# Performance work log

Measured on AMD Instinct MI355X. Metric: run time of the kernel, lower is better.

Reference implementation:

```python
import jax, jax.numpy as jnp
import numpy as np
from jax import lax

D_MODEL = 1024
D_STATE = 128
HEADDIM = 64
EXPAND = 2
NGROUPS = 1
CHUNK = 256
D_INNER = EXPAND * D_MODEL          # 2048
D_SSM = D_INNER                      # d_ssm defaults to d_inner
NHEADS = D_SSM // HEADDIM            # 32
CONV_DIM = D_SSM + 2 * NGROUPS * D_STATE   # 2304
D_IN_PROJ = 2 * D_INNER + 2 * NGROUPS * D_STATE + NHEADS  # 4384 -> d_mlp = 0
BATCH = 2
SEQLEN = 2048
EPS = 1e-5


def setup_inputs() -> dict:
    key = jax.random.key(0)
    ks = jax.random.split(key, 9)
    u = jax.random.normal(ks[0], (BATCH, SEQLEN, D_MODEL), jnp.float32)
    # indices into left-padded (len = SEQLEN+1) sequence; 0 selects the zero pad
    conv_indices = jax.random.randint(ks[1], (BATCH, 4 * SEQLEN), 0, SEQLEN + 1)
    W_in = jax.random.normal(ks[2], (D_IN_PROJ, D_MODEL), jnp.float32) / np.sqrt(D_MODEL).astype(np.float32)
    conv_w = jax.random.normal(ks[3], (CONV_DIM, 4), jnp.float32) * 0.2
    conv_b = jax.random.normal(ks[4], (CONV_DIM,), jnp.float32) * 0.02
    # dt_bias init exactly as the module: inverse-softplus of dt in [dt_min, dt_max]
    dt = jnp.exp(jax.random.uniform(ks[5], (NHEADS,), jnp.float32) * (np.log(0.1) - np.log(0.001)) + np.log(0.001))
    dt = jnp.clip(dt, 1e-4)
    dt_bias = dt + jnp.log(-jnp.expm1(-dt))
    A_log = jnp.log(jax.random.uniform(ks[6], (NHEADS,), jnp.float32, minval=1.0, maxval=16.0))
    D = jnp.ones((NHEADS,), jnp.float32)
    norm_w = jnp.ones((D_SSM,), jnp.float32)
    W_out = jax.random.normal(ks[7], (D_MODEL, D_INNER), jnp.float32) / np.sqrt(D_INNER).astype(np.float32)
    return dict(u=u, conv_indices=conv_indices, W_in=W_in, conv_w=conv_w, conv_b=conv_b,
                dt_bias=dt_bias, A_log=A_log, D=D, norm_w=norm_w, W_out=W_out)


def _segsum(x):
    # x: (b, c, h, cs) -> (b, c, h, cs, cs); out[..., t, s] = sum_{k=s+1..t} x[..., k]
    cs = x.shape[-1]
    cx = jnp.cumsum(x, axis=-1)
    diff = cx[..., :, None] - cx[..., None, :]
    mask = jnp.tril(jnp.ones((cs, cs), dtype=bool))
    return jnp.where(mask, diff, -jnp.inf)


def _ssd(x, dt, A, Bh, Ch, D):
    # Mamba2 SSD chunked scan. x:(b,l,h,p), dt:(b,l,h), A:(h,), Bh/Ch:(b,l,h,n), D:(h,)
    b, l, h, p = x.shape
    n = Bh.shape[-1]
    c = l // CHUNK
    xr = x.reshape(b, c, CHUNK, h, p)
    dtr = dt.reshape(b, c, CHUNK, h)
    Br = Bh.reshape(b, c, CHUNK, h, n)
    Cr = Ch.reshape(b, c, CHUNK, h, n)
    dA = dtr * A                                 # (b,c,cs,h)
    Acum = jnp.cumsum(dA, axis=2)                # (b,c,cs,h)
    Lm = jnp.exp(_segsum(jnp.transpose(dA, (0, 1, 3, 2))))  # (b,c,h,cs,cs)
    dtx = xr * dtr[..., None]                    # dt-weighted inputs
    # intra-chunk (diagonal blocks)
    Yd = jnp.einsum('bcthn,bcshn,bchts,bcshp->bcthp', Cr, Br, Lm, dtx)
    # per-chunk final states
    decay_states = jnp.exp(Acum[:, :, -1:, :] - Acum)        # (b,c,cs,h)
    states = jnp.einsum('bcshn,bcsh,bcshp->bchpn', Br, decay_states, dtx)
    chunk_decay = jnp.exp(Acum[:, :, -1, :])     # (b,c,h)
    def step(h_prev, inp):
        dec, st = inp
        return h_prev * dec[..., None, None] + st, h_prev
    init = jnp.zeros((b, h, p, n), x.dtype)
    _, prev = lax.scan(step, init, (jnp.moveaxis(chunk_decay, 1, 0), jnp.moveaxis(states, 1, 0)))
    prev = jnp.moveaxis(prev, 0, 1)              # (b,c,h,p,n): state entering each chunk
    # inter-chunk (off-diagonal) contribution
    Yoff = jnp.einsum('bcthn,bchpn,bcth->bcthp', Cr, prev, jnp.exp(Acum))
    Y = Yd + Yoff + D[None, None, None, :, None] * xr
    return Y.reshape(b, l, h, p)


def reference(u, conv_indices, W_in, conv_w, conv_b, dt_bias, A_log, D, norm_w, W_out):
    b, l, _ = u.shape
    zxbcdt = u @ W_in.T                          # (b,l,4384); d_mlp == 0
    z, xBC, dt_raw = jnp.split(zxbcdt, [D_SSM, D_SSM + CONV_DIM], axis=-1)
    # tree conv: left-pad seq by 1, gather 4 tree positions per output step, depthwise conv k=4 stride=4
    xc = jnp.transpose(xBC, (0, 2, 1))           # (b, conv_dim, l)
    xp = jnp.pad(xc, ((0, 0), (0, 0), (1, 0)))
    idx = jnp.broadcast_to(conv_indices[:, None, :], (b, CONV_DIM, 4 * l))
    g = jnp.take_along_axis(xp, idx, axis=2).reshape(b, CONV_DIM, l, 4)
    conv = jnp.einsum('bclk,ck->bcl', g, conv_w) + conv_b[None, :, None]
    xBC = jax.nn.silu(jnp.transpose(conv, (0, 2, 1)))  # (b,l,conv_dim)
    x, Bm, Cm = jnp.split(xBC, [D_SSM, D_SSM + NGROUPS * D_STATE], axis=-1)
    x = x.reshape(b, l, NHEADS, HEADDIM)
    hpg = NHEADS // NGROUPS
    Bh = jnp.repeat(Bm.reshape(b, l, NGROUPS, D_STATE), hpg, axis=2)
    Ch = jnp.repeat(Cm.reshape(b, l, NGROUPS, D_STATE), hpg, axis=2)
    dt = jax.nn.softplus(dt_raw + dt_bias)       # dt_softplus=True, default dt_limit
    A = -jnp.exp(A_log.astype(jnp.float32))
    y = _ssd(x, dt, A, Bh, Ch, D).reshape(b, l, D_SSM)
    # RMSNormGated, norm_before_gate=False, group_size = d_ssm (ngroups=1)
    yz = y * jax.nn.silu(z)
    var = jnp.mean(jnp.square(yz), axis=-1, keepdims=True)
    y = yz * lax.rsqrt(var + EPS) * norm_w
    return y @ W_out.T
```

## Files before the change

### kernel.cpp

```cpp
#include <hip/hip_runtime.h>

#define BB 2
#define LL 2048
#define DMODEL 1024
#define DSSM 2048
#define NH 32
#define HD 64
#define DST 128
#define CONVD 2304
#define DPROJ 4384
#define CS 64
#define NC 32
#define BLTOT (BB*LL)

typedef short v8s __attribute__((ext_vector_type(8)));
typedef float v4f __attribute__((ext_vector_type(4)));

__device__ __forceinline__ float b2f(unsigned short h) {
  union { unsigned int u; float f; } v; v.u = ((unsigned int)h) << 16; return v.f;
}
__device__ __forceinline__ unsigned short f2b(float f) {
  union { float f; unsigned int u; } v; v.f = f;
  unsigned int u = v.u;
  return (unsigned short)((u + 0x7fffu + ((u >> 16) & 1u)) >> 16);
}
__device__ __forceinline__ v4f mfma16(v8s a, v8s b, v4f c) {
  return __builtin_amdgcn_mfma_f32_16x16x32_bf16(a, b, c, 0, 0, 0);
}
__device__ __forceinline__ void gl_lds16(const unsigned short* g, unsigned short* l) {
  __builtin_amdgcn_global_load_lds(
      (const __attribute__((address_space(1))) void*)(g),
      (__attribute__((address_space(3))) void*)(l), 16, 0, 0);
}

__global__ __launch_bounds__(256) void cvt3_kernel(
    const float* __restrict__ a, unsigned short* __restrict__ oa, int na4,
    const float* __restrict__ b, unsigned short* __restrict__ ob, int nb4,
    const float* __restrict__ c, unsigned short* __restrict__ oc, int nc4)
{
  int i = blockIdx.x * 256 + threadIdx.x;
  const float* src; unsigned short* dst; int j;
  if (i < na4) { src = a; dst = oa; j = i; }
  else if (i < na4 + nb4) { src = b; dst = ob; j = i - na4; }
  else if (i < na4 + nb4 + nc4) { src = c; dst = oc; j = i - na4 - nb4; }
  else return;
  float4 v = ((const float4*)src)[j];
  ushort4 o;
  o.x = f2b(v.x); o.y = f2b(v.y); o.z = f2b(v.z); o.w = f2b(v.w);
  ((ushort4*)dst)[j] = o;
}

template<int TN, int OUT_BF16>
__global__ __launch_bounds__(256) void gemm_bt(
    const unsigned short* __restrict__ A, const unsigned short* __restrict__ Bt,
    void* __restrict__ Cout, int M, int N, int K, int ldc)
{
  constexpr int NT = TN / 32;
  const int bm = blockIdx.x, bn = blockIdx.y;
  const int tid = threadIdx.x;
  const int wave = tid >> 6, lane = tid & 63;
  const int wm = wave & 1, wn = wave >> 1;
  const int q = lane >> 4, lr = lane & 15;

  __shared__ __align__(16) unsigned short smem[128 * 64 + TN * 64];
  unsigned short* As = smem;
  unsigned short* Bs = smem + 128 * 64;

  v4f acc[4][NT];
#pragma unroll
  for (int i = 0; i < 4; i++)
#pragma unroll
    for (int j = 0; j < NT; j++) acc[i][j] = v4f{0.f, 0.f, 0.f, 0.f};

  const int lrow = lane >> 3;
  const int gchunk = (lane & 7) ^ lrow;

  for (int k0 = 0; k0 < K; k0 += 64) {
    __syncthreads();
#pragma unroll
    for (int it = 0; it < 4; ++it) {
      int r = wave * 32 + it * 8 + lrow;
      gl_lds16(A + (size_t)(bm * 128 + r) * K + k0 + gchunk * 8,
               &As[(wave * 32 + it * 8) * 64]);
    }
#pragma unroll
    for (int it = 0; it < TN / 32; ++it) {
      int rloc = wave * (TN / 4) + it * 8;
      int rb = bn * TN + rloc + lrow; if (rb >= N) rb = N - 1;
      gl_lds16(Bt + (size_t)rb * K + k0 + gchunk * 8, &Bs[rloc * 64]);
    }
    __syncthreads();
#pragma unroll
    for (int ks = 0; ks < 64; ks += 32) {
      const int c0 = (ks >> 3) + q;
      v8s af[4], bf[NT];
#pragma unroll
      for (int mt = 0; mt < 4; ++mt) {
        int r = wm * 64 + mt * 16 + lr;
        af[mt] = *(const v8s*)&As[r * 64 + ((c0 ^ (r & 7)) << 3)];
      }
#pragma unroll
      for (int nt = 0; nt < NT; ++nt) {
        int r = wn * (TN / 2) + nt * 16 + lr;
        bf[nt] = *(const v8s*)&Bs[r * 64 + ((c0 ^ (r & 7)) << 3)];
      }
#pragma unroll
      for (int mt = 0; mt < 4; ++mt)
#pragma unroll
        for (int nt = 0; nt < NT; ++nt)
          acc[mt][nt] = mfma16(af[mt], bf[nt], acc[mt][nt]);
    }
  }

  if constexpr (OUT_BF16) {
    __syncthreads();
    unsigned short* Cs = smem;
#pragma unroll
    for (int mt = 0; mt < 4; ++mt) {
#pragma unroll
      for (int nt = 0; nt < NT; ++nt) {
        int col = wn * (TN / 2) + nt * 16 + lr;
#pragma unroll
        for (int r = 0; r < 4; ++r) {
          int row = wm * 64 + mt * 16 + q * 4 + r;
          int baddr = (row * (TN * 2) + col * 2) ^ ((row & 7) << 4);
          *(unsigned short*)((char*)Cs + baddr) = f2b(acc[mt][nt][r]);
        }
      }
    }
    __syncthreads();
    constexpr int CHR = TN / 8;
#pragma unroll
    for (int u = tid; u < 128 * CHR; u += 256) {
      int row = u / CHR, ch = u % CHR;
      int baddr = row * (TN * 2) + ((ch ^ (row & 7)) << 4);
      uint4 v = *(const uint4*)((const char*)Cs + baddr);
      int gcol = bn * TN + ch * 8;
      if (gcol < N)
        *(uint4*)((unsigned short*)Cout + (size_t)(bm * 128 + row) * ldc + gcol) = v;
    }
  } else {
#pragma unroll
    for (int mt = 0; mt < 4; ++mt) {
#pragma unroll
      for (int nt = 0; nt < NT; ++nt) {
        int row = bm * 128 + wm * 64 + mt * 16 + q * 4;
        int col = bn * TN + wn * (TN / 2) + nt * 16 + lr;
        if (col < N) {
#pragma unroll
          for (int r = 0; r < 4; ++r)
            ((float*)Cout)[(size_t)(row + r) * ldc + col] = acc[mt][nt][r];
        }
      }
    }
  }
}

__global__ __launch_bounds__(256) void convBC_kernel(
    const unsigned short* __restrict__ C1, const int* __restrict__ cidx,
    const float* __restrict__ convw, const float* __restrict__ convb,
    const float* __restrict__ dtbias,
    unsigned short* __restrict__ Bg16, unsigned short* __restrict__ Cg16,
    float* __restrict__ dtb)
{
  int bl0 = blockIdx.x * 16;
  int b = bl0 >> 11;
  int tid = threadIdx.x;
  __shared__ int idxs[64];
  if (tid < 64) {
    int tk = tid >> 2, k = tid & 3;
    idxs[tid] = cidx[b * (4 * LL) + (((bl0 + tk) & 2047) * 4) + k];
  }
  __syncthreads();
  const float4* cw4 = (const float4*)convw;
  int quad = tid & 63;
  int relc = DSSM + quad * 4;
  float4 w0 = cw4[relc], w1 = cw4[relc + 1], w2 = cw4[relc + 2], w3 = cw4[relc + 3];
  float4 cb = *(const float4*)(convb + relc);
  int tk0 = (tid >> 6) * 4;
#pragma unroll
  for (int tt = 0; tt < 4; ++tt) {
    int tk = tk0 + tt;
    int bl = bl0 + tk;
    ushort4 rv[4];
#pragma unroll
    for (int k = 0; k < 4; ++k) {
      int iv = idxs[tk * 4 + k];
      rv[k] = (iv > 0) ? *(const ushort4*)(C1 + (size_t)(b * LL + iv - 1) * DPROJ + DSSM + relc)
                       : make_ushort4(0, 0, 0, 0);
    }
    float a0 = cb.x + b2f(rv[0].x) * w0.x + b2f(rv[1].x) * w0.y + b2f(rv[2].x) * w0.z + b2f(rv[3].x) * w0.w;
    float a1 = cb.y + b2f(rv[0].y) * w1.x + b2f(rv[1].y) * w1.y + b2f(rv[2].y) * w1.z + b2f(rv[3].y) * w1.w;
    float a2 = cb.z + b2f(rv[0].z) * w2.x + b2f(rv[1].z) * w2.y + b2f(rv[2].z) * w2.z + b2f(rv[3].z) * w2.w;
    float a3 = cb.w + b2f(rv[0].w) * w3.x + b2f(rv[1].w) * w3.y + b2f(rv[2].w) * w3.z + b2f(rv[3].w) * w3.w;
    ushort4 o;
    o.x = f2b(a0 / (1.f + __expf(-a0)));
    o.y = f2b(a1 / (1.f + __expf(-a1)));
    o.z = f2b(a2 / (1.f + __expf(-a2)));
    o.w = f2b(a3 / (1.f + __expf(-a3)));
    int cc = relc - DSSM;
    if (cc < DST) *(ushort4*)(Bg16 + (size_t)bl * DST + cc) = o;
    else          *(ushort4*)(Cg16 + (size_t)bl * DST + (cc - DST)) = o;
  }
  for (int u = tid; u < 16 * NH; u += 256) {
    int tk = u >> 5, hh = u & 31;
    int bl = bl0 + tk;
    float raw = b2f(C1[(size_t)bl * DPROJ + DSSM + CONVD + hh]) + dtbias[hh];
    float dtv = (raw > 20.f) ? raw : log1pf(__expf(raw));
    dtb[(size_t)bl * NH + hh] = dtv;
  }
}

__global__ __launch_bounds__(256) void d1_intra(
    const unsigned short* __restrict__ C1, const int* __restrict__ cidx,
    const float* __restrict__ convw, const float* __restrict__ convb,
    const unsigned short* __restrict__ Bg16,
    const unsigned short* __restrict__ Cg16, const float* __restrict__ dtb,
    const float* __restrict__ A_log, const float* __restrict__ Dp,
    unsigned short* __restrict__ y16, unsigned short* __restrict__ statesb,
    float* __restrict__ cdb, float* __restrict__ acumb)
{
  int gid = blockIdx.x;
  int h = gid & 31, ci = (gid >> 5) & 31, b = gid >> 10;
  int tid = threadIdx.x, wave = tid >> 6, lane = tid & 63, q = lane >> 4, lr = lane & 15;

  __shared__ __align__(16) unsigned short BnG[CS * 136];
  __shared__ __align__(16) unsigned short BTw[DST * 72];
  __shared__ __align__(16) unsigned short xT[HD * 72];
  __shared__ float dt_s[CS], ac_s[CS], dec_s[CS];
  __shared__ int idxs[CS * 4];
  __shared__ float wls[HD * 4];
  __shared__ float bls[HD];

  const size_t blbase = (size_t)b * LL + ci * CS;
  const size_t chbase = (size_t)(b * NC + ci) * NH + h;
  float Ah = -__expf(A_log[h]);

  if (wave == 0) {
    float d = dtb[(blbase + lane) * NH + h];
    float a = d * Ah;
#pragma unroll
    for (int off = 1; off < 64; off <<= 1) {
      float u = __shfl_up(a, off, 64);
      if (lane >= off) a += u;
    }
    float tot = __shfl(a, 63, 64);
    dt_s[lane] = d;
    ac_s[lane] = a;
    dec_s[lane] = __expf(tot - a);
    acumb[chbase * CS + lane] = a;
    if (lane == 0) cdb[chbase] = __expf(tot);
  }

#pragma unroll
  for (int g = 0; g < 8; ++g) {
    int f = g * 256 + tid;
    int s = f >> 5, c4 = (f & 31) * 4;
    *(ushort4*)&BnG[s * 136 + c4] = *(const ushort4*)(Bg16 + (blbase + s) * DST + c4);
  }
  {
    int s = tid >> 2, k = tid & 3;
    idxs[tid] = cidx[b * (4 * LL) + (ci * CS + s) * 4 + k];
  }
  if (tid < HD) *(float4*)&wls[tid * 4] = *(const float4*)(convw + (h * HD + tid) * 4);
  if (tid < HD / 4) *(float4*)&bls[tid * 4] = *(const float4*)(convb + h * HD + tid * 4);
  __syncthreads();

#pragma unroll
  for (int g = 0; g < 4; ++g) {
    int f = g * 256 + tid;
    int n = f >> 3, sg = f & 7;
    int s0 = sg * 8;
    ushort4 lo, hi;
    lo.x = f2b(b2f(BnG[(s0 + 0) * 136 + n]) * dec_s[s0 + 0] * dt_s[s0 + 0]);
    lo.y = f2b(b2f(BnG[(s0 + 1) * 136 + n]) * dec_s[s0 + 1] * dt_s[s0 + 1]);
    lo.z = f2b(b2f(BnG[(s0 + 2) * 136 + n]) * dec_s[s0 + 2] * dt_s[s0 + 2]);
    lo.w = f2b(b2f(BnG[(s0 + 3) * 136 + n]) * dec_s[s0 + 3] * dt_s[s0 + 3]);
    hi.x = f2b(b2f(BnG[(s0 + 4) * 136 + n]) * dec_s[s0 + 4] * dt_s[s0 + 4]);
    hi.y = f2b(b2f(BnG[(s0 + 5) * 136 + n]) * dec_s[s0 + 5] * dt_s[s0 + 5]);
    hi.z = f2b(b2f(BnG[(s0 + 6) * 136 + n]) * dec_s[s0 + 6] * dt_s[s0 + 6]);
    hi.w = f2b(b2f(BnG[(s0 + 7) * 136 + n]) * dec_s[s0 + 7] * dt_s[s0 + 7]);
    *(ushort4*)&BTw[n * 72 + s0] = lo;
    *(ushort4*)&BTw[n * 72 + s0 + 4] = hi;
  }

  v4f accS[4];
#pragma unroll
  for (int i = 0; i < 4; i++) accS[i] = v4f{0.f, 0.f, 0.f, 0.f};
#pragma unroll
  for (int ks = 0; ks < 128; ks += 32) {
    v8s a = *(const v8s*)(Cg16 + (blbase + wave * 16 + lr) * DST + ks + q * 8);
#pragma unroll
    for (int si = 0; si < 4; ++si) {
      v8s bb = *(const v8s*)&BnG[(si * 16 + lr) * 136 + ks + q * 8];
      accS[si] = mfma16(a, bb, accS[si]);
    }
  }

#pragma unroll
  for (int g = 0; g < 4; ++g) {
    int f = g * 256 + tid;
    int s = f >> 4, p4 = (f & 15) * 4;
    ushort4 rv[4];
#pragma unroll
    for (int k = 0; k < 4; ++k) {
      int iv = idxs[s * 4 + k];
      rv[k] = (iv > 0) ? *(const ushort4*)(C1 + (size_t)(b * LL + iv - 1) * DPROJ + DSSM + h * HD + p4)
                       : make_ushort4(0, 0, 0, 0);
    }
    float4 w0 = *(const float4*)&wls[(p4 + 0) * 4];
    float4 w1 = *(const float4*)&wls[(p4 + 1) * 4];
    float4 w2 = *(const float4*)&wls[(p4 + 2) * 4];
    float4 w3 = *(const float4*)&wls[(p4 + 3) * 4];
    float a0 = bls[p4 + 0] + b2f(rv[0].x) * w0.x + b2f(rv[1].x) * w0.y + b2f(rv[2].x) * w0.z + b2f(rv[3].x) * w0.w;
    float a1 = bls[p4 + 1] + b2f(rv[0].y) * w1.x + b2f(rv[1].y) * w1.y + b2f(rv[2].y) * w1.z + b2f(rv[3].y) * w1.w;
    float a2 = bls[p4 + 2] + b2f(rv[0].z) * w2.x + b2f(rv[1].z) * w2.y + b2f(rv[2].z) * w2.z + b2f(rv[3].z) * w2.w;
    float a3 = bls[p4 + 3] + b2f(rv[0].w) * w3.x + b2f(rv[1].w) * w3.y + b2f(rv[2].w) * w3.z + b2f(rv[3].w) * w3.w;
    xT[(p4 + 0) * 72 + s] = f2b(a0 / (1.f + __expf(-a0)));
    xT[(p4 + 1) * 72 + s] = f2b(a1 / (1.f + __expf(-a1)));
    xT[(p4 + 2) * 72 + s] = f2b(a2 / (1.f + __expf(-a2)));
    xT[(p4 + 3) * 72 + s] = f2b(a3 / (1.f + __expf(-a3)));
  }
  __syncthreads();

  {
    int tbase = wave * 16 + q * 4;
#pragma unroll
    for (int si = 0; si < 4; ++si) {
      int s = si * 16 + lr;
      float ds = dt_s[s], as = ac_s[s];
#pragma unroll
      for (int r = 0; r < 4; ++r) {
        int tt = tbase + r;
        float g = 0.f;
        if (s <= tt) g = accS[si][r] * __expf(ac_s[tt] - as) * ds;
        BnG[tt * 72 + s] = f2b(g);
      }
    }
  }
  __syncthreads();

  v4f accY[4], accPT[4][2];
#pragma unroll
  for (int i = 0; i < 4; i++) {
    accY[i] = v4f{0.f,0.f,0.f,0.f};
    accPT[i][0] = v4f{0.f,0.f,0.f,0.f};
    accPT[i][1] = v4f{0.f,0.f,0.f,0.f};
  }
  int nw = wave * 32;
#pragma unroll
  for (int ks = 0; ks < 64; ks += 32) {
    v8s xf[4];
#pragma unroll
    for (int i = 0; i < 4; ++i) xf[i] = *(const v8s*)&xT[(i * 16 + lr) * 72 + ks + q * 8];
    v8s aG  = *(const v8s*)&BnG[(wave * 16 + lr) * 72 + ks + q * 8];
    v8s bw0 = *(const v8s*)&BTw[(nw + lr) * 72 + ks + q * 8];
    v8s bw1 = *(const v8s*)&BTw[(nw + 16 + lr) * 72 + ks + q * 8];
#pragma unroll
    for (int nt = 0; nt < 4; ++nt) {
      accY[nt] = mfma16(aG, xf[nt], accY[nt]);
      accPT[nt][0] = mfma16(xf[nt], bw0, accPT[nt][0]);
      accPT[nt][1] = mfma16(xf[nt], bw1, accPT[nt][1]);
    }
  }

  float Dh = Dp[h];
#pragma unroll
  for (int nt = 0; nt < 4; ++nt) {
    int p = nt * 16 + lr;
#pragma unroll
    for (int r = 0; r < 4; ++r) {
      int t = wave * 16 + q * 4 + r;
      float xv = b2f(xT[p * 72 + t]);
      y16[(blbase + t) * DSSM + h * HD + p] = f2b(accY[nt][r] + Dh * xv);
    }
  }
  size_t sbase = chbase * (DST * HD);
#pragma unroll
  for (int mt = 0; mt < 4; ++mt) {
#pragma unroll
    for (int nt = 0; nt < 2; ++nt) {
      int n = nw + nt * 16 + lr;
#pragma unroll
      for (int r = 0; r < 4; ++r) {
        int p = mt * 16 + q * 4 + r;
        statesb[sbase + (size_t)p * DST + n] = f2b(accPT[mt][nt][r]);
      }
    }
  }
}

__global__ __launch_bounds__(256) void d2_scan(
    unsigned short* __restrict__ statesb, const float* __restrict__ cdb)
{
  int g = blockIdx.x;
  int seg = g & 31, bh = g >> 5;
  int b = bh >> 5, h = bh & 31;
  int e = seg * 256 + threadIdx.x;
  const size_t cstride = (size_t)NH * DST * HD;
  size_t base = ((size_t)(b * NC) * NH + h) * (DST * HD) + e;
  unsigned short st[NC];
#pragma unroll
  for (int ci = 0; ci < NC; ++ci) st[ci] = statesb[base + ci * cstride];
  float run = 0.f;
#pragma unroll
  for (int ci = 0; ci < NC; ++ci) {
    float cd = cdb[(b * NC + ci) * NH + h];
    statesb[base + ci * cstride] = f2b(run);
    run = run * cd + b2f(st[ci]);
  }
}

__global__ __launch_bounds__(256) void d3_inter(
    const unsigned short* __restrict__ Cg16,
    const unsigned short* __restrict__ statesb, const float* __restrict__ acumb,
    unsigned short* __restrict__ y16)
{
  int gid = blockIdx.x;
  int h = gid & 31, ci = (gid >> 5) & 31, b = gid >> 10;
  int tid = threadIdx.x, wave = tid >> 6, lane = tid & 63, q = lane >> 4, lr = lane & 15;
  __shared__ __align__(16) unsigned short pT[HD * 136];
  __shared__ __align__(16) float ys[CS * 68];
  __shared__ float ea[CS];
  const size_t blbase = (size_t)b * LL + ci * CS;
  const size_t chbase = (size_t)(b * NC + ci) * NH + h;
  if (tid < CS) ea[tid] = __expf(acumb[chbase * CS + tid]);
  size_t sbase = chbase * (DST * HD);
#pragma unroll
  for (int g = 0; g < 8; ++g) {
    int f = g * 256 + tid;
    int p = f >> 5, c4 = (f & 31) * 4;
    *(ushort4*)&pT[p * 136 + c4] = *(const ushort4*)(statesb + sbase + (size_t)p * DST + c4);
  }
  __syncthreads();
  v4f acc[4];
#pragma unroll
  for (int i = 0; i < 4; i++) acc[i] = v4f{0.f, 0.f, 0.f, 0.f};
#pragma unroll
  for (int ks = 0; ks < 128; ks += 32) {
    v8s a = *(const v8s*)(Cg16 + (blbase + wave * 16 + lr) * DST + ks + q * 8);
#pragma unroll
    for (int nt = 0; nt < 4; ++nt) {
      v8s bb = *(const v8s*)&pT[(nt * 16 + lr) * 136 + ks + q * 8];
      acc[nt] = mfma16(a, bb, acc[nt]);
    }
  }
#pragma unroll
  for (int nt = 0; nt < 4; ++nt) {
#pragma unroll
    for (int r = 0; r < 4; ++r)
      ys[(wave * 16 + q * 4 + r) * 68 + nt * 16 + lr] = acc[nt][r];
  }
  __syncthreads();
#pragma unroll
  for (int it = 0; it < 2; ++it) {
    int unit = it * 256 + tid;
    int t = unit >> 3, p8 = (unit & 7) * 8;
    float ea_t = ea[t];
    size_t off = (blbase + t) * DSSM + h * HD + p8;
    uint4 yv = *(const uint4*)(y16 + off);
    float4 o0 = *(const float4*)&ys[t * 68 + p8];
    float4 o1 = *(const float4*)&ys[t * 68 + p8 + 4];
    const unsigned int* yu = (const unsigned int*)&yv;
    float oo[8] = {o0.x, o0.y, o0.z, o0.w, o1.x, o1.y, o1.z, o1.w};
    unsigned int ro[4];
#pragma unroll
    for (int d = 0; d < 4; ++d) {
      unsigned short y0 = (unsigned short)(yu[d] & 0xffffu), y1 = (unsigned short)(yu[d] >> 16);
      float v0 = b2f(y0) + ea_t * oo[d * 2 + 0];
      float v1 = b2f(y1) + ea_t * oo[d * 2 + 1];
      ro[d] = (unsigned int)f2b(v0) | ((unsigned int)f2b(v1) << 16);
    }
    *(uint4*)(y16 + off) = make_uint4(ro[0], ro[1], ro[2], ro[3]);
  }
}

__global__ __launch_bounds__(256) void norm_kernel(
    const unsigned short* __restrict__ y16, const unsigned short* __restrict__ C1,
    const float* __restrict__ normw, unsigned short* __restrict__ yzn)
{
  int bl = blockIdx.x;
  int tid = threadIdx.x;
  int wave = tid >> 6, lane = tid & 63;
  int c8 = tid * 8;
  uint4 yv = *(const uint4*)(y16 + (size_t)bl * DSSM + c8);
  uint4 zv = *(const uint4*)(C1 + (size_t)bl * DPROJ + c8);
  const unsigned int* yu = (const unsigned int*)&yv;
  const unsigned int* zu = (const unsigned int*)&zv;
  float vals[8];
  float ss = 0.f;
#pragma unroll
  for (int d = 0; d < 4; ++d) {
    unsigned short y0 = (unsigned short)(yu[d] & 0xffffu), y1 = (unsigned short)(yu[d] >> 16);
    unsigned short z0 = (unsigned short)(zu[d] & 0xffffu), z1 = (unsigned short)(zu[d] >> 16);
    float zf0 = b2f(z0), zf1 = b2f(z1);
    float v0 = b2f(y0) * (zf0 / (1.f + __expf(-zf0)));
    float v1 = b2f(y1) * (zf1 / (1.f + __expf(-zf1)));
    vals[d * 2] = v0; vals[d * 2 + 1] = v1;
    ss += v0 * v0 + v1 * v1;
  }
#pragma unroll
  for (int off = 32; off > 0; off >>= 1) ss += __shfl_down(ss, off);
  __shared__ float red[4];
  if (lane == 0) red[wave] = ss;
  __syncthreads();
  float tot = red[0] + red[1] + red[2] + red[3];
  float scale = rsqrtf(tot * (1.f / 2048.f) + 1e-5f);
  float4 w0 = *(const float4*)(normw + c8);
  float4 w1 = *(const float4*)(normw + c8 + 4);
  float ws[8] = {w0.x, w0.y, w0.z, w0.w, w1.x, w1.y, w1.z, w1.w};
  unsigned int ro[4];
#pragma unroll
  for (int d = 0; d < 4; ++d) {
    unsigned short r0 = f2b(vals[d * 2] * scale * ws[d * 2]);
    unsigned short r1 = f2b(vals[d * 2 + 1] * scale * ws[d * 2 + 1]);
    ro[d] = (unsigned int)r0 | ((unsigned int)r1 << 16);
  }
  *(uint4*)(yzn + (size_t)bl * DSSM + c8) = make_uint4(ro[0], ro[1], ro[2], ro[3]);
}

extern "C" void kernel_launch(void* const* d_in, const int* in_sizes, int n_in,
                              void* d_out, int out_size, void* d_ws, size_t ws_size,
                              hipStream_t stream) {
  const float* u      = (const float*)d_in[0];
  const int*   cidx   = (const int*)d_in[1];
  const float* W_in   = (const float*)d_in[2];
  const float* convw  = (const float*)d_in[3];
  const float* convb  = (const float*)d_in[4];
  const float* dtbias = (const float*)d_in[5];
  const float* A_log  = (const float*)d_in[6];
  const float* Dp     = (const float*)d_in[7];
  const float* normw  = (const float*)d_in[8];
  const float* W_out  = (const float*)d_in[9];

  char* w = (char*)d_ws;
  size_t off = 0;
  auto alloc = [&](size_t bytes) { char* p = w + off; off += (bytes + 255) & ~(size_t)255; return p; };
  unsigned short* u16     = (unsigned short*)alloc((size_t)BLTOT * DMODEL * 2);
  unsigned short* Win16   = (unsigned short*)alloc((size_t)DPROJ * DMODEL * 2);
  unsigned short* Wout16  = (unsigned short*)alloc((size_t)DMODEL * DSSM * 2);
  unsigned short* C1      = (unsigned short*)alloc((size_t)BLTOT * DPROJ * 2);
  unsigned short* Bg16    = (unsigned short*)alloc((size_t)BLTOT * DST * 2);
  unsigned short* Cg16    = (unsigned short*)alloc((size_t)BLTOT * DST * 2);
  float*          dtb     = (float*)alloc((size_t)BLTOT * NH * 4);
  float*          acumb   = (float*)alloc((size_t)BB * NC * NH * CS * 4);
  unsigned short* y16     = (unsigned short*)alloc((size_t)BLTOT * DSSM * 2);
  unsigned short* statesb = (unsigned short*)alloc((size_t)BB * NC * NH * DST * HD * 2);
  float*          cdb     = (float*)alloc((size_t)BB * NC * NH * 4);
  unsigned short* yzn     = (unsigned short*)alloc((size_t)BLTOT * DSSM * 2);

  const int na4 = BLTOT * DMODEL / 4, nb4 = DPROJ * DMODEL / 4, nc4 = DMODEL * DSSM / 4;
  cvt3_kernel<<<(na4 + nb4 + nc4 + 255) / 256, 256, 0, stream>>>(
      u, u16, na4, W_in, Win16, nb4, W_out, Wout16, nc4);

  gemm_bt<128, 1><<<dim3(BLTOT / 128, (DPROJ + 127) / 128), 256, 0, stream>>>(
      u16, Win16, C1, BLTOT, DPROJ, DMODEL, DPROJ);
  convBC_kernel<<<BLTOT / 16, 256, 0, stream>>>(C1, cidx, convw, convb, dtbias, Bg16, Cg16, dtb);
  d1_intra<<<BB * NC * NH, 256, 0, stream>>>(C1, cidx, convw, convb, Bg16, Cg16, dtb,
                                             A_log, Dp, y16, statesb, cdb, acumb);
  d2_scan<<<BB * NH * 32, 256, 0, stream>>>(statesb, cdb);
  d3_inter<<<BB * NC * NH, 256, 0, stream>>>(Cg16, statesb, acumb, y16);
  norm_kernel<<<BLTOT, 256, 0, stream>>>(y16, C1, normw, yzn);
  gemm_bt<64, 0><<<dim3(BLTOT / 128, DMODEL / 64), 256, 0, stream>>>(
      yzn, Wout16, (float*)d_out, BLTOT, DMODEL, DSSM, DMODEL);
}
```

Measured before the change: 262.8 us.

## Double-buffer GEMM LDS tiles and simplify bf16 epilogue to direct stores

Splits the GEMM shared-memory tiles into two buffers and prefetches the next K tile with direct global-to-LDS loads while MFMAs run on the current one, leaving one wait+barrier per iteration. The aim is to hide global load latency behind compute. The bf16 output path also drops its LDS-staged coalesced write and stores scalar bf16 values straight to global memory. That makes the writes narrower and less coalesced, and doubling LDS use may lower occupancy.

```diff
diff --git a/kernel.cpp b/kernel.cpp
--- a/kernel.cpp
+++ b/kernel.cpp
@@ -62,9 +62,8 @@
   const int wm = wave & 1, wn = wave >> 1;
   const int q = lane >> 4, lr = lane & 15;
 
-  __shared__ __align__(16) unsigned short smem[128 * 64 + TN * 64];
-  unsigned short* As = smem;
-  unsigned short* Bs = smem + 128 * 64;
+  __shared__ __align__(16) unsigned short As[2][128 * 64];
+  __shared__ __align__(16) unsigned short Bs[2][TN * 64];
 
   v4f acc[4][NT];
 #pragma unroll
@@ -75,21 +74,35 @@
   const int lrow = lane >> 3;
   const int gchunk = (lane & 7) ^ lrow;
 
-  for (int k0 = 0; k0 < K; k0 += 64) {
-    __syncthreads();
-#pragma unroll
-    for (int it = 0; it < 4; ++it) {
-      int r = wave * 32 + it * 8 + lrow;
-      gl_lds16(A + (size_t)(bm * 128 + r) * K + k0 + gchunk * 8,
-               &As[(wave * 32 + it * 8) * 64]);
-    }
-#pragma unroll
-    for (int it = 0; it < TN / 32; ++it) {
-      int rloc = wave * (TN / 4) + it * 8;
-      int rb = bn * TN + rloc + lrow; if (rb >= N) rb = N - 1;
-      gl_lds16(Bt + (size_t)rb * K + k0 + gchunk * 8, &Bs[rloc * 64]);
-    }
-    __syncthreads();
+#define STAGE_TILE(bufi, k0) do {                                              \
+    _Pragma("unroll")                                                          \
+    for (int it = 0; it < 4; ++it) {                                           \
+      int r = wave * 32 + it * 8 + lrow;                                       \
+      gl_lds16(A + (size_t)(bm * 128 + r) * K + (k0) + gchunk * 8,             \
+               &As[bufi][(wave * 32 + it * 8) * 64]);                          \
+    }                                                                          \
+    _Pragma("unroll")                                                          \
+    for (int it = 0; it < TN / 32; ++it) {                                     \
+      int rloc = wave * (TN / 4) + it * 8;                                     \
+      int rb = bn * TN + rloc + lrow; if (rb >= N) rb = N - 1;                 \
+      gl_lds16(Bt + (size_t)rb * K + (k0) + gchunk * 8, &Bs[bufi][rloc * 64]); \
+    }                                                                          \
+  } while (0)
+
+#define WAIT_BARRIER() do {                                                    \
+    __builtin_amdgcn_sched_barrier(0);                                         \
+    asm volatile("s_waitcnt vmcnt(0) lgkmcnt(0)\ns_barrier" ::: "memory");     \
+  } while (0)
+
+  const int nkt = K >> 6;
+  STAGE_TILE(0, 0);
+  WAIT_BARRIER();
+
+  for (int kt = 0; kt < nkt; ++kt) {
+    const int cb = kt & 1;
+    if (kt + 1 < nkt) STAGE_TILE(cb ^ 1, (kt + 1) << 6);
+    const unsigned short* __restrict__ Ab = As[cb];
+    const unsigned short* __restrict__ Bb = Bs[cb];
 #pragma unroll
     for (int ks = 0; ks < 64; ks += 32) {
       const int c0 = (ks >> 3) + q;
@@ -97,12 +110,12 @@
 #pragma unroll
       for (int mt = 0; mt < 4; ++mt) {
         int r = wm * 64 + mt * 16 + lr;
-        af[mt] = *(const v8s*)&As[r * 64 + ((c0 ^ (r & 7)) << 3)];
+        af[mt] = *(const v8s*)&Ab[r * 64 + ((c0 ^ (r & 7)) << 3)];
       }
 #pragma unroll
       for (int nt = 0; nt < NT; ++nt) {
         int r = wn * (TN / 2) + nt * 16 + lr;
-        bf[nt] = *(const v8s*)&Bs[r * 64 + ((c0 ^ (r & 7)) << 3)];
+        bf[nt] = *(const v8s*)&Bb[r * 64 + ((c0 ^ (r & 7)) << 3)];
       }
 #pragma unroll
       for (int mt = 0; mt < 4; ++mt)
@@ -110,46 +123,23 @@
         for (int nt = 0; nt < NT; ++nt)
           acc[mt][nt] = mfma16(af[mt], bf[nt], acc[mt][nt]);
     }
-  }
-
-  if constexpr (OUT_BF16) {
-    __syncthreads();
-    unsigned short* Cs = smem;
-#pragma unroll
-    for (int mt = 0; mt < 4; ++mt) {
-#pragma unroll
-      for (int nt = 0; nt < NT; ++nt) {
-        int col = wn * (TN / 2) + nt * 16 + lr;
+    if (kt + 1 < nkt) WAIT_BARRIER();
+  }
+#undef STAGE_TILE
+#undef WAIT_BARRIER
+
+#pragma unroll
+  for (int mt = 0; mt < 4; ++mt) {
+#pragma unroll
+    for (int nt = 0; nt < NT; ++nt) {
+      int row = bm * 128 + wm * 64 + mt * 16 + q * 4;
+      int col = bn * TN + wn * (TN / 2) + nt * 16 + lr;
+      if (col < N) {
 #pragma unroll
         for (int r = 0; r < 4; ++r) {
-          int row = wm * 64 + mt * 16 + q * 4 + r;
-          int baddr = (row * (TN * 2) + col * 2) ^ ((row & 7) << 4);
-          *(unsigned short*)((char*)Cs + baddr) = f2b(acc[mt][nt][r]);
-        }
-      }
-    }
-    __syncthreads();
-    constexpr int CHR = TN / 8;
-#pragma unroll
-    for (int u = tid; u < 128 * CHR; u += 256) {
-      int row = u / CHR, ch = u % CHR;
-      int baddr = row * (TN * 2) + ((ch ^ (row & 7)) << 4);
-      uint4 v = *(const uint4*)((const char*)Cs + baddr);
-      int gcol = bn * TN + ch * 8;
-      if (gcol < N)
-        *(uint4*)((unsigned short*)Cout + (size_t)(bm * 128 + row) * ldc + gcol) = v;
-    }
-  } else {
-#pragma unroll
-    for (int mt = 0; mt < 4; ++mt) {
-#pragma unroll
-      for (int nt = 0; nt < NT; ++nt) {
-        int row = bm * 128 + wm * 64 + mt * 16 + q * 4;
-        int col = bn * TN + wn * (TN / 2) + nt * 16 + lr;
-        if (col < N) {
-#pragma unroll
-          for (int r = 0; r < 4; ++r)
-            ((float*)Cout)[(size_t)(row + r) * ldc + col] = acc[mt][nt][r];
+          float v = acc[mt][nt][r];
+          if (OUT_BF16) ((unsigned short*)Cout)[(size_t)(row + r) * ldc + col] = f2b(v);
+          else          ((float*)Cout)[(size_t)(row + r) * ldc + col] = v;
         }
       }
     }
```

Result: no change. 267.6 us (+1.8%).
